# Kernel optimization log

Measured on AMD Instinct MI355X. Metric: run time of the kernel, lower is better.

The kernel has to match this reference:

```python
import jax, jax.numpy as jnp
import numpy as np

N_LEVELS = 16
F_PER_LEVEL = 2
LOG2_T = 19
T = 1 << LOG2_T            # 524288 entries per level
BASE_RES = 16
PER_LEVEL_SCALE = 1.3819
HIDDEN = 64
DIM = 3
PRIMES = (1, 2654435761, 805459861)  # tcnn spatial hash primes

# 8 corner offsets of the unit cube, shape (8, 3)
_CORNERS = np.stack(np.meshgrid(*([np.array([0, 1])] * DIM), indexing='ij'), -1).reshape(-1, DIM)


def hashgrid_encode(x01, table):
    """x01: (N,3) in [0,1]; table: (L, T, F). Returns (N, L*F)."""
    offs = jnp.asarray(_CORNERS, dtype=jnp.int32)          # (8,3)
    offs_u = offs.astype(jnp.uint32)
    feats = []
    for lvl in range(N_LEVELS):
        scale = BASE_RES * (PER_LEVEL_SCALE ** lvl) - 1.0   # grid scale (tcnn convention)
        res = int(np.ceil(scale)) + 1                       # grid resolution for this level
        pos = x01 * jnp.float32(scale) + 0.5
        p0 = jnp.floor(pos)
        w = pos - p0                                        # (N,3) trilinear weights
        p0i = p0.astype(jnp.int32)
        corner = p0i[:, None, :] + offs[None]               # (N,8,3)
        if res ** DIM <= T:
            # dense (coarse) level: linear indexing
            idx = corner[..., 0] + corner[..., 1] * res + corner[..., 2] * (res * res)
        else:
            # fine level: xor spatial hash modulo table size
            c = p0i[:, None, :].astype(jnp.uint32) + offs_u[None]
            h = (c[..., 0] * jnp.uint32(PRIMES[0])) ^ (c[..., 1] * jnp.uint32(PRIMES[1])) ^ (c[..., 2] * jnp.uint32(PRIMES[2]))
            idx = (h & jnp.uint32(T - 1)).astype(jnp.int32)
        cf = table[lvl][idx]                                # (N,8,F) irregular gather
        # trilinear weight per corner: prod over dims of (w if offset==1 else 1-w)
        wmask = jnp.where(offs[None] == 1, w[:, None, :], 1.0 - w[:, None, :])  # (N,8,3)
        wc = jnp.prod(wmask, axis=-1)                       # (N,8)
        feats.append(jnp.sum(cf * wc[..., None], axis=1))   # (N,F)
    return jnp.concatenate(feats, axis=-1)                  # (N, 32)


def _xavier(key, fan_in, fan_out):
    lim = jnp.sqrt(6.0 / (fan_in + fan_out))
    return jax.random.uniform(key, (fan_in, fan_out), jnp.float32, -lim, lim)


def setup_inputs() -> dict:
    key = jax.random.key(0)
    k = jax.random.split(key, 8)
    x = jax.random.uniform(k[0], (1048576, DIM), jnp.float32, -1.0, 1.0)
    # tcnn hashgrid init: uniform(-1e-4, 1e-4)
    table = jax.random.uniform(k[1], (N_LEVELS, T, F_PER_LEVEL), jnp.float32, -1e-4, 1e-4)
    in_dim = N_LEVELS * F_PER_LEVEL
    W1 = _xavier(k[2], in_dim, HIDDEN); b1 = jnp.zeros((HIDDEN,), jnp.float32)
    W2 = _xavier(k[3], HIDDEN, HIDDEN); b2 = jnp.zeros((HIDDEN,), jnp.float32)
    W3 = _xavier(k[4], HIDDEN, 1);      b3 = jnp.zeros((1,), jnp.float32)
    return {"x": x, "table": table, "W1": W1, "b1": b1, "W2": W2, "b2": b2, "W3": W3, "b3": b3}


def reference(x, table, W1, b1, W2, b2, W3, b3):
    x01 = (x + 1.0) * 0.5                       # map [-1,1] -> [0,1]
    enc = hashgrid_encode(x01, table)           # (N, 32)
    h = jax.nn.relu(enc @ W1 + b1)
    h = jax.nn.relu(h @ W2 + b2)
    h = h @ W3 + b3                             # (N, 1), clip_sdf is None
    return h
```

## Files before the change

kernel.cpp:

```cpp
#include <hip/hip_runtime.h>
#include <hip/hip_fp16.h>
#include <cstdint>

#define NTHREADS 256
#define TBL_SIZE (1u << 19)
#define HIDDEN 64
#define NLVL 16
#define PPT 2
#define ENC_SCALE 256.0f
#define ENC_INV (1.0f / 256.0f)

struct Levels { float scale[16]; int res[16]; int dense[16]; };
constexpr Levels make_levels() {
    Levels L{};
    double s = 16.0;
    for (int l = 0; l < 16; ++l) {
        double sc = s - 1.0;
        L.scale[l] = (float)sc;
        int fi = (int)sc;
        int res = fi + (((double)fi < sc) ? 1 : 0) + 1;
        L.res[l] = res;
        L.dense[l] = ((long long)res * res * res <= (long long)TBL_SIZE) ? 1 : 0;
        s *= 1.3819;
    }
    return L;
}
constexpr Levels LV = make_levels();

struct PairOffs { int off[17]; int total; };
constexpr PairOffs make_pairoffs() {
    PairOffs P{}; int o = 0;
    for (int l = 0; l < 16; ++l) {
        P.off[l] = o;
        if (LV.dense[l]) {
            const int r = LV.res[l];
            o += r * (1 + r + r * r) + 2;
        }
    }
    P.off[16] = o; P.total = o;
    return P;
}
constexpr PairOffs PO = make_pairoffs();

#define H16(M) M(0) M(1) M(2) M(3) M(4) M(5) M(6) M(7) \
               M(8) M(9) M(10) M(11) M(12) M(13) M(14) M(15)

typedef _Float16 f16x8 __attribute__((ext_vector_type(8)));
typedef float f32x4 __attribute__((ext_vector_type(4)));

static __device__ __forceinline__ __half2 u32_h2(uint32_t u) {
    union { uint32_t u; __half2 h; } c; c.u = u; return c.h;
}

__global__ __launch_bounds__(256) void cvt_table(const float2* __restrict__ in,
                                                 __half2* __restrict__ out, int n) {
    for (int i = blockIdx.x * 256 + threadIdx.x; i < n; i += gridDim.x * 256) {
        const float2 v = in[i];
        out[i] = __floats2half2_rn(v.x, v.y);
    }
}

__global__ __launch_bounds__(256) void cvt_quads(const __half2* __restrict__ h2,
                                                 uint4* __restrict__ qd) {
    for (int i = blockIdx.x * 256 + threadIdx.x; i < PO.total; i += gridDim.x * 256) {
        int lvl = 0;
        #pragma unroll
        for (int l = 0; l < NLVL; ++l)
            if (LV.dense[l] && i >= PO.off[l] && i < PO.off[l + 1]) lvl = l;
        const int local = i - PO.off[lvl];
        const int res = LV.res[lvl];
        const uint32_t* base = reinterpret_cast<const uint32_t*>(h2 + (size_t)lvl * TBL_SIZE + local);
        uint4 q;
        q.x = base[0];
        q.y = base[1];
        q.z = base[res];
        q.w = base[res + 1];
        qd[i] = q;
    }
}

__global__ __launch_bounds__(256) void cvt_wfrags(const float* __restrict__ W1,
                                                  const float* __restrict__ W2,
                                                  __half* __restrict__ w1f,
                                                  __half* __restrict__ w2f) {
    const int t = blockIdx.x * 256 + threadIdx.x;
    for (int i = t; i < 4 * 64 * 8; i += gridDim.x * 256) {
        const int j = i & 7, lane = (i >> 3) & 63, nt = i >> 9;
        const int k = (lane >> 4) * 8 + j;
        const int o = (lane & 15) + 16 * nt;
        w1f[i] = __float2half(W1[k * HIDDEN + o]);
    }
    for (int i = t; i < 4 * 2 * 64 * 8; i += gridDim.x * 256) {
        const int j = i & 7, lane = (i >> 3) & 63, kb = (i >> 9) & 1, nt = i >> 10;
        const int k = 32 * kb + (lane >> 4) * 8 + j;
        const int o = (lane & 15) + 16 * nt;
        w2f[i] = __float2half(W2[k * HIDDEN + o]);
    }
}

static __device__ __forceinline__ float2 gather_level(
    const __half2* __restrict__ tl, const uint4* __restrict__ qd,
    int dense, int res, int doff,
    int iu, int iv, int iw, float wu, float wv, float ww)
{
    float f0 = 0.0f, f1 = 0.0f;
    const float lx = 1.0f - wu;
    if (dense) {
        const int base = iu + iv * res + iw * res * res;
        #pragma unroll
        for (int o2 = 0; o2 < 2; ++o2) {
            const int idx = base + (o2 ? res * res : 0);
            const uint4 q = qd[doff + idx];
            const float2 a = __half22float2(u32_h2(q.x));
            const float2 b = __half22float2(u32_h2(q.y));
            const float2 c = __half22float2(u32_h2(q.z));
            const float2 d = __half22float2(u32_h2(q.w));
            const float x0l = fmaf(lx, a.x, wu * b.x);
            const float x1l = fmaf(lx, c.x, wu * d.x);
            const float y0l = fmaf(lx, a.y, wu * b.y);
            const float y1l = fmaf(lx, c.y, wu * d.y);
            const float bil0 = fmaf(1.0f - wv, x0l, wv * x1l);
            const float bil1 = fmaf(1.0f - wv, y0l, wv * y1l);
            const float wz = o2 ? ww : 1.0f - ww;
            f0 = fmaf(bil0, wz, f0);
            f1 = fmaf(bil1, wz, f1);
        }
    } else {
        const uint32_t r1a = (uint32_t)iv * 2654435761u;
        const uint32_t r1b = r1a + 2654435761u;
        const uint32_t r2a = (uint32_t)iw * 805459861u;
        const uint32_t r2b = r2a + 805459861u;
        if ((iu & 1) == 0) {
            #pragma unroll
            for (int b4 = 0; b4 < 4; ++b4) {
                const int o1 = (b4 >> 1) & 1, o2 = b4 & 1;
                const uint32_t rest = (o1 ? r1b : r1a) ^ (o2 ? r2b : r2a);
                const uint32_t h0 = ((uint32_t)iu ^ rest) & (TBL_SIZE - 1u);
                const unsigned long long pr =
                    *reinterpret_cast<const unsigned long long*>(tl + (h0 & ~1u));
                const uint32_t lo = (uint32_t)pr, hi = (uint32_t)(pr >> 32);
                const uint32_t sel = h0 & 1u;
                const float2 a = __half22float2(u32_h2(sel ? hi : lo));
                const float2 b = __half22float2(u32_h2(sel ? lo : hi));
                const float wyz = (o1 ? wv : 1.0f - wv) * (o2 ? ww : 1.0f - ww);
                f0 = fmaf(fmaf(lx, a.x, wu * b.x), wyz, f0);
                f1 = fmaf(fmaf(lx, a.y, wu * b.y), wyz, f1);
            }
        } else {
            #pragma unroll
            for (int b4 = 0; b4 < 4; ++b4) {
                const int o1 = (b4 >> 1) & 1, o2 = b4 & 1;
                const uint32_t rest = (o1 ? r1b : r1a) ^ (o2 ? r2b : r2a);
                const uint32_t h0 = ((uint32_t)iu ^ rest) & (TBL_SIZE - 1u);
                const uint32_t h1 = ((uint32_t)(iu + 1) ^ rest) & (TBL_SIZE - 1u);
                const float2 a = __half22float2(tl[h0]);
                const float2 b = __half22float2(tl[h1]);
                const float wyz = (o1 ? wv : 1.0f - wv) * (o2 ? ww : 1.0f - ww);
                f0 = fmaf(fmaf(lx, a.x, wu * b.x), wyz, f0);
                f1 = fmaf(fmaf(lx, a.y, wu * b.y), wyz, f1);
            }
        }
    }
    return make_float2(f0, f1);
}

__global__ __launch_bounds__(NTHREADS, 8) void encode_phased(
    const float* __restrict__ x,
    const __half2* __restrict__ tbl,
    const uint4* __restrict__ qd,
    __half2* __restrict__ enc, int n, int nb)
{
    const int bid = blockIdx.x;
    const int lvl = bid / nb;
    const int pb  = bid - lvl * nb;
    const int i0 = pb * (NTHREADS * PPT) + threadIdx.x;
    const int i1 = i0 + NTHREADS;
    if (i0 >= n) return;

    const float sc = LV.scale[lvl];
    const int res = LV.res[lvl];
    const int dense = LV.dense[lvl];
    const int doff = PO.off[lvl];
    const __half2* tl = tbl + (size_t)lvl * TBL_SIZE;

    const float u0 = (x[3 * i0 + 0] + 1.0f) * 0.5f;
    const float v0 = (x[3 * i0 + 1] + 1.0f) * 0.5f;
    const float w0 = (x[3 * i0 + 2] + 1.0f) * 0.5f;
    const float pu0 = u0 * sc + 0.5f, pv0 = v0 * sc + 0.5f, pw0 = w0 * sc + 0.5f;
    const float fu0 = floorf(pu0), fv0 = floorf(pv0), fw0 = floorf(pw0);

    const bool has1 = (i1 < n);
    const int j1 = has1 ? i1 : i0;
    const float u1 = (x[3 * j1 + 0] + 1.0f) * 0.5f;
    const float v1 = (x[3 * j1 + 1] + 1.0f) * 0.5f;
    const float w1 = (x[3 * j1 + 2] + 1.0f) * 0.5f;
    const float pu1 = u1 * sc + 0.5f, pv1 = v1 * sc + 0.5f, pw1 = w1 * sc + 0.5f;
    const float fu1 = floorf(pu1), fv1 = floorf(pv1), fw1 = floorf(pw1);

    const float2 fA = gather_level(tl, qd, dense, res, doff,
                                   (int)fu0, (int)fv0, (int)fw0,
                                   pu0 - fu0, pv0 - fv0, pw0 - fw0);
    const float2 fB = gather_level(tl, qd, dense, res, doff,
                                   (int)fu1, (int)fv1, (int)fw1,
                                   pu1 - fu1, pv1 - fv1, pw1 - fw1);

    enc[(size_t)lvl * n + i0] = __floats2half2_rn(fA.x * ENC_SCALE, fA.y * ENC_SCALE);
    if (has1) enc[(size_t)lvl * n + i1] = __floats2half2_rn(fB.x * ENC_SCALE, fB.y * ENC_SCALE);
}

__global__ __launch_bounds__(256) void mlp_mfma(
    const __half2* __restrict__ enc,
    const __half* __restrict__ w1f, const __half* __restrict__ w2f,
    const float* __restrict__ b1, const float* __restrict__ b2,
    const float* __restrict__ W3, const float* __restrict__ b3,
    float* __restrict__ out, int n)
{
    __shared__ __half lds_h1[4][64][18];
    const int wid  = threadIdx.x >> 6;
    const int lane = threadIdx.x & 63;
    const int tile = blockIdx.x * 4 + wid;
    const int pt = lane & 15;
    const int qw = lane >> 4;
    const int i = tile * 16 + pt;

    union { uint32_t u[4]; f16x8 v; } bf;
    #pragma unroll
    for (int jj = 0; jj < 4; ++jj)
        bf.u[jj] = *reinterpret_cast<const uint32_t*>(&enc[(size_t)(qw * 4 + jj) * n + i]);

    f32x4 c1[4];
    #pragma unroll
    for (int nt = 0; nt < 4; ++nt) {
        const float4 bb = *(const float4*)&b1[16 * nt + qw * 4];
        c1[nt][0] = bb.x * ENC_SCALE; c1[nt][1] = bb.y * ENC_SCALE;
        c1[nt][2] = bb.z * ENC_SCALE; c1[nt][3] = bb.w * ENC_SCALE;
        const f16x8 a = *reinterpret_cast<const f16x8*>(&w1f[(nt * 64 + lane) * 8]);
        c1[nt] = __builtin_amdgcn_mfma_f32_16x16x32_f16(a, bf.v, c1[nt], 0, 0, 0);
    }

    #pragma unroll
    for (int nt = 0; nt < 4; ++nt) {
        #pragma unroll
        for (int r = 0; r < 4; ++r) {
            const int o = 16 * nt + qw * 4 + r;
            lds_h1[wid][o][pt] = __float2half(fmaxf(c1[nt][r], 0.0f));
        }
    }

    f32x4 c2[4];
    #pragma unroll
    for (int nt = 0; nt < 4; ++nt) {
        const float4 bb = *(const float4*)&b2[16 * nt + qw * 4];
        c2[nt][0] = bb.x * ENC_SCALE; c2[nt][1] = bb.y * ENC_SCALE;
        c2[nt][2] = bb.z * ENC_SCALE; c2[nt][3] = bb.w * ENC_SCALE;
    }
    #pragma unroll
    for (int kb = 0; kb < 2; ++kb) {
        union { uint32_t u[4]; f16x8 v; } hb;
        #pragma unroll
        for (int j2 = 0; j2 < 4; ++j2) {
            const int k0 = kb * 32 + qw * 8 + 2 * j2;
            const uint32_t lo = __half_as_ushort(lds_h1[wid][k0][pt]);
            const uint32_t hi = __half_as_ushort(lds_h1[wid][k0 + 1][pt]);
            hb.u[j2] = lo | (hi << 16);
        }
        #pragma unroll
        for (int nt = 0; nt < 4; ++nt) {
            const f16x8 a = *reinterpret_cast<const f16x8*>(&w2f[((nt * 2 + kb) * 64 + lane) * 8]);
            c2[nt] = __builtin_amdgcn_mfma_f32_16x16x32_f16(a, hb.v, c2[nt], 0, 0, 0);
        }
    }

    float part = 0.0f;
    #pragma unroll
    for (int nt = 0; nt < 4; ++nt) {
        const float4 w3v = *(const float4*)&W3[16 * nt + qw * 4];
        part = fmaf(fmaxf(c2[nt][0], 0.0f), w3v.x, part);
        part = fmaf(fmaxf(c2[nt][1], 0.0f), w3v.y, part);
        part = fmaf(fmaxf(c2[nt][2], 0.0f), w3v.z, part);
        part = fmaf(fmaxf(c2[nt][3], 0.0f), w3v.w, part);
    }
    part += __shfl_xor(part, 16, 64);
    part += __shfl_xor(part, 32, 64);
    if (lane < 16) out[i] = part * ENC_INV + b3[0];
}

__global__ __launch_bounds__(NTHREADS, 4) void mlp_kernel(
    const __half2* __restrict__ enc,
    const float* __restrict__ W1, const float* __restrict__ b1,
    const float* __restrict__ W2, const float* __restrict__ b2,
    const float* __restrict__ W3, const float* __restrict__ b3,
    float* __restrict__ out, int n)
{
    const int i = blockIdx.x * NTHREADS + threadIdx.x;
    if (i >= n) return;

#define DECLH(m) float4 h##m = *(const float4*)&b1[4 * (m)];
    H16(DECLH)
#undef DECLH

    #pragma unroll
    for (int l = 0; l < NLVL; ++l) {
        const float2 f = __half22float2(enc[(size_t)l * n + i]);
        const float f0 = f.x * ENC_INV, f1 = f.y * ENC_INV;
        const float* wra = &W1[(2 * l) * HIDDEN];
        const float* wrb = &W1[(2 * l + 1) * HIDDEN];
#define UPDH(m) { \
        const float4 wa = *(const float4*)&wra[4 * (m)]; \
        const float4 wb = *(const float4*)&wrb[4 * (m)]; \
        h##m.x = fmaf(f0, wa.x, fmaf(f1, wb.x, h##m.x)); \
        h##m.y = fmaf(f0, wa.y, fmaf(f1, wb.y, h##m.y)); \
        h##m.z = fmaf(f0, wa.z, fmaf(f1, wb.z, h##m.z)); \
        h##m.w = fmaf(f0, wa.w, fmaf(f1, wb.w, h##m.w)); }
        H16(UPDH)
#undef UPDH
    }

#define RELUH(m) { h##m.x = fmaxf(h##m.x, 0.0f); h##m.y = fmaxf(h##m.y, 0.0f); \
                   h##m.z = fmaxf(h##m.z, 0.0f); h##m.w = fmaxf(h##m.w, 0.0f); }
    H16(RELUH)
#undef RELUH

    float acc = b3[0];
    #pragma unroll 2
    for (int jb = 0; jb < HIDDEN; jb += 4) {
        float4 t = *(const float4*)&b2[jb];
#define L2K(m) { \
        const float4 r0 = *(const float4*)&W2[(4 * (m) + 0) * HIDDEN + jb]; \
        const float4 r1 = *(const float4*)&W2[(4 * (m) + 1) * HIDDEN + jb]; \
        const float4 r2 = *(const float4*)&W2[(4 * (m) + 2) * HIDDEN + jb]; \
        const float4 r3 = *(const float4*)&W2[(4 * (m) + 3) * HIDDEN + jb]; \
        t.x = fmaf(h##m.x, r0.x, t.x); t.y = fmaf(h##m.x, r0.y, t.y); \
        t.z = fmaf(h##m.x, r0.z, t.z); t.w = fmaf(h##m.x, r0.w, t.w); \
        t.x = fmaf(h##m.y, r1.x, t.x); t.y = fmaf(h##m.y, r1.y, t.y); \
        t.z = fmaf(h##m.y, r1.z, t.z); t.w = fmaf(h##m.y, r1.w, t.w); \
        t.x = fmaf(h##m.z, r2.x, t.x); t.y = fmaf(h##m.z, r2.y, t.y); \
        t.z = fmaf(h##m.z, r2.z, t.z); t.w = fmaf(h##m.z, r2.w, t.w); \
        t.x = fmaf(h##m.w, r3.x, t.x); t.y = fmaf(h##m.w, r3.y, t.y); \
        t.z = fmaf(h##m.w, r3.z, t.z); t.w = fmaf(h##m.w, r3.w, t.w); }
        H16(L2K)
#undef L2K
        const float4 w3v = *(const float4*)&W3[jb];
        acc = fmaf(fmaxf(t.x, 0.0f), w3v.x, acc);
        acc = fmaf(fmaxf(t.y, 0.0f), w3v.y, acc);
        acc = fmaf(fmaxf(t.z, 0.0f), w3v.z, acc);
        acc = fmaf(fmaxf(t.w, 0.0f), w3v.w, acc);
    }

    out[i] = acc;
}

template <bool USE_H2>
__global__ __launch_bounds__(NTHREADS, 4) void sdf_tcnn_fused(
    const float* __restrict__ x,
    const void* __restrict__ tbl,
    const float* __restrict__ W1, const float* __restrict__ b1,
    const float* __restrict__ W2, const float* __restrict__ b2,
    const float* __restrict__ W3, const float* __restrict__ b3,
    float* __restrict__ out, int n)
{
    const int i = blockIdx.x * NTHREADS + threadIdx.x;
    if (i >= n) return;

    const float u = (x[3 * i + 0] + 1.0f) * 0.5f;
    const float v = (x[3 * i + 1] + 1.0f) * 0.5f;
    const float w = (x[3 * i + 2] + 1.0f) * 0.5f;

#define DECLH(m) float4 h##m = *(const float4*)&b1[4 * (m)];
    H16(DECLH)
#undef DECLH

    #pragma unroll
    for (int l = 0; l < NLVL; ++l) {
        const float sc = LV.scale[l];
        const int res = LV.res[l];
        const float pu = u * sc + 0.5f;
        const float pv = v * sc + 0.5f;
        const float pw = w * sc + 0.5f;
        const float fu = floorf(pu), fv = floorf(pv), fw = floorf(pw);
        const float wu = pu - fu, wv = pv - fv, ww = pw - fw;
        const int iu = (int)fu, iv = (int)fv, iw = (int)fw;

        int idx[8];
        #pragma unroll
        for (int b = 0; b < 8; ++b) {
            const int o0 = (b >> 2) & 1, o1 = (b >> 1) & 1, o2 = b & 1;
            if (LV.dense[l]) {
                idx[b] = (iu + o0) + (iv + o1) * res + (iw + o2) * (res * res);
            } else {
                const uint32_t c0 = (uint32_t)(iu + o0);
                const uint32_t c1 = (uint32_t)(iv + o1);
                const uint32_t c2 = (uint32_t)(iw + o2);
                const uint32_t h = c0 ^ (c1 * 2654435761u) ^ (c2 * 805459861u);
                idx[b] = (int)(h & (TBL_SIZE - 1u));
            }
        }

        float f0 = 0.0f, f1 = 0.0f;
        if constexpr (USE_H2) {
            const __half2* tl = (const __half2*)tbl + (size_t)l * TBL_SIZE;
            __half2 cfh[8];
            #pragma unroll
            for (int b = 0; b < 8; ++b) cfh[b] = tl[idx[b]];
            #pragma unroll
            for (int b = 0; b < 8; ++b) {
                const int o0 = (b >> 2) & 1, o1 = (b >> 1) & 1, o2 = b & 1;
                const float wt = (o0 ? wu : 1.0f - wu) *
                                 (o1 ? wv : 1.0f - wv) *
                                 (o2 ? ww : 1.0f - ww);
                const float2 cf = __half22float2(cfh[b]);
                f0 = fmaf(cf.x, wt, f0);
                f1 = fmaf(cf.y, wt, f1);
            }
        } else {
            const float2* tl = (const float2*)tbl + (size_t)l * TBL_SIZE;
            float2 cf[8];
            #pragma unroll
            for (int b = 0; b < 8; ++b) cf[b] = tl[idx[b]];
            #pragma unroll
            for (int b = 0; b < 8; ++b) {
                const int o0 = (b >> 2) & 1, o1 = (b >> 1) & 1, o2 = b & 1;
                const float wt = (o0 ? wu : 1.0f - wu) *
                                 (o1 ? wv : 1.0f - wv) *
                                 (o2 ? ww : 1.0f - ww);
                f0 = fmaf(cf[b].x, wt, f0);
                f1 = fmaf(cf[b].y, wt, f1);
            }
        }

        const float* wra = &W1[(2 * l) * HIDDEN];
        const float* wrb = &W1[(2 * l + 1) * HIDDEN];
#define UPDH(m) { \
        const float4 wa = *(const float4*)&wra[4 * (m)]; \
        const float4 wb = *(const float4*)&wrb[4 * (m)]; \
        h##m.x = fmaf(f0, wa.x, fmaf(f1, wb.x, h##m.x)); \
        h##m.y = fmaf(f0, wa.y, fmaf(f1, wb.y, h##m.y)); \
        h##m.z = fmaf(f0, wa.z, fmaf(f1, wb.z, h##m.z)); \
        h##m.w = fmaf(f0, wa.w, fmaf(f1, wb.w, h##m.w)); }
        H16(UPDH)
#undef UPDH
    }

#define RELUH(m) { h##m.x = fmaxf(h##m.x, 0.0f); h##m.y = fmaxf(h##m.y, 0.0f); \
                   h##m.z = fmaxf(h##m.z, 0.0f); h##m.w = fmaxf(h##m.w, 0.0f); }
    H16(RELUH)
#undef RELUH

    float acc = b3[0];
    #pragma unroll 2
    for (int jb = 0; jb < HIDDEN; jb += 4) {
        float4 t = *(const float4*)&b2[jb];
#define L2K(m) { \
        const float4 r0 = *(const float4*)&W2[(4 * (m) + 0) * HIDDEN + jb]; \
        const float4 r1 = *(const float4*)&W2[(4 * (m) + 1) * HIDDEN + jb]; \
        const float4 r2 = *(const float4*)&W2[(4 * (m) + 2) * HIDDEN + jb]; \
        const float4 r3 = *(const float4*)&W2[(4 * (m) + 3) * HIDDEN + jb]; \
        t.x = fmaf(h##m.x, r0.x, t.x); t.y = fmaf(h##m.x, r0.y, t.y); \
        t.z = fmaf(h##m.x, r0.z, t.z); t.w = fmaf(h##m.x, r0.w, t.w); \
        t.x = fmaf(h##m.y, r1.x, t.x); t.y = fmaf(h##m.y, r1.y, t.y); \
        t.z = fmaf(h##m.y, r1.z, t.z); t.w = fmaf(h##m.y, r1.w, t.w); \
        t.x = fmaf(h##m.z, r2.x, t.x); t.y = fmaf(h##m.z, r2.y, t.y); \
        t.z = fmaf(h##m.z, r2.z, t.z); t.w = fmaf(h##m.z, r2.w, t.w); \
        t.x = fmaf(h##m.w, r3.x, t.x); t.y = fmaf(h##m.w, r3.y, t.y); \
        t.z = fmaf(h##m.w, r3.z, t.z); t.w = fmaf(h##m.w, r3.w, t.w); }
        H16(L2K)
#undef L2K
        const float4 w3v = *(const float4*)&W3[jb];
        acc = fmaf(fmaxf(t.x, 0.0f), w3v.x, acc);
        acc = fmaf(fmaxf(t.y, 0.0f), w3v.y, acc);
        acc = fmaf(fmaxf(t.z, 0.0f), w3v.z, acc);
        acc = fmaf(fmaxf(t.w, 0.0f), w3v.w, acc);
    }

    out[i] = acc;
}

extern "C" void kernel_launch(void* const* d_in, const int* in_sizes, int n_in,
                              void* d_out, int out_size, void* d_ws, size_t ws_size,
                              hipStream_t stream) {
    const float* x     = (const float*)d_in[0];
    const float* table = (const float*)d_in[1];
    const float* W1    = (const float*)d_in[2];
    const float* b1    = (const float*)d_in[3];
    const float* W2    = (const float*)d_in[4];
    const float* b2    = (const float*)d_in[5];
    const float* W3    = (const float*)d_in[6];
    const float* b3    = (const float*)d_in[7];
    float* out = (float*)d_out;

    const int n = in_sizes[0] / 3;
    const int n_entries = NLVL * (int)TBL_SIZE;
    const size_t tbl_bytes   = (size_t)n_entries * sizeof(__half2);
    const size_t quad_bytes  = (size_t)PO.total * 16;
    const size_t wfrag_bytes = 16384;
    const size_t enc_bytes   = (size_t)NLVL * (size_t)n * sizeof(__half2);
    const int nb_mlp = (n + NTHREADS - 1) / NTHREADS;
    const int nb_enc = (n + NTHREADS * PPT - 1) / (NTHREADS * PPT);

    if (ws_size >= tbl_bytes + quad_bytes + wfrag_bytes + enc_bytes) {
        __half2* tbl_h2 = (__half2*)d_ws;
        uint4* qd = (uint4*)((char*)d_ws + tbl_bytes);
        __half* w1f = (__half*)((char*)d_ws + tbl_bytes + quad_bytes);
        __half* w2f = w1f + 4 * 64 * 8;
        __half2* enc = (__half2*)((char*)d_ws + tbl_bytes + quad_bytes + wfrag_bytes);

        hipLaunchKernelGGL(cvt_table, dim3(2048), dim3(256), 0, stream,
                           (const float2*)table, tbl_h2, n_entries);
        hipLaunchKernelGGL(cvt_quads, dim3((PO.total + 255) / 256), dim3(256), 0, stream,
                           tbl_h2, qd);
        hipLaunchKernelGGL(cvt_wfrags, dim3(16), dim3(256), 0, stream,
                           W1, W2, w1f, w2f);
        hipLaunchKernelGGL(encode_phased, dim3(nb_enc * NLVL), dim3(NTHREADS), 0, stream,
                           x, tbl_h2, qd, enc, n, nb_enc);
        if ((n & 63) == 0) {
            hipLaunchKernelGGL(mlp_mfma, dim3(n / 64), dim3(256), 0, stream,
                               enc, w1f, w2f, b1, b2, W3, b3, out, n);
        } else {
            hipLaunchKernelGGL(mlp_kernel, dim3(nb_mlp), dim3(NTHREADS), 0, stream,
                               enc, W1, b1, W2, b2, W3, b3, out, n);
        }
    } else if (ws_size >= tbl_bytes) {
        __half2* tbl_h2 = (__half2*)d_ws;
        hipLaunchKernelGGL(cvt_table, dim3(2048), dim3(256), 0, stream,
                           (const float2*)table, tbl_h2, n_entries);
        hipLaunchKernelGGL((sdf_tcnn_fused<true>), dim3(nb_mlp), dim3(NTHREADS), 0, stream,
                           x, (const void*)tbl_h2, W1, b1, W2, b2, W3, b3, out, n);
    } else {
        hipLaunchKernelGGL((sdf_tcnn_fused<false>), dim3(nb_mlp), dim3(NTHREADS), 0, stream,
                           x, (const void*)table, W1, b1, W2, b2, W3, b3, out, n);
    }
}
```

Before: 334.3 us.

## Split dense and hash level encoding, skip fp16 conversion of dense table levels

Dense levels now get their fp16 corner quads straight from the fp32 table, so the full-table fp16 conversion only covers the hashed levels. The five dense levels are encoded in one kernel that reads each point's coordinates once and loops over levels, while hashed levels keep the per-level phased kernel. The scalar MLP fallback and the intermediate fp16-only fused path are removed, and mlp_mfma is launched with a rounded-up grid even when n is not a multiple of 64. The aim is to cut conversion traffic and launch and x-read overhead, at the cost of an extra launch and fewer blocks for the dense kernel.

```diff
diff --git a/kernel.cpp b/kernel.cpp
--- a/kernel.cpp
+++ b/kernel.cpp
@@ -6,6 +6,8 @@
 #define TBL_SIZE (1u << 19)
 #define HIDDEN 64
 #define NLVL 16
+#define NDENSE 5
+#define NHASH (NLVL - NDENSE)
 #define PPT 2
 #define ENC_SCALE 256.0f
 #define ENC_INV (1.0f / 256.0f)
@@ -26,6 +28,7 @@
     return L;
 }
 constexpr Levels LV = make_levels();
+static_assert(LV.dense[NDENSE - 1] == 1 && LV.dense[NDENSE] == 0, "dense split");
 
 struct PairOffs { int off[17]; int total; };
 constexpr PairOffs make_pairoffs() {
@@ -51,6 +54,9 @@
 static __device__ __forceinline__ __half2 u32_h2(uint32_t u) {
     union { uint32_t u; __half2 h; } c; c.u = u; return c.h;
 }
+static __device__ __forceinline__ uint32_t h2_u32(__half2 h) {
+    union { __half2 h; uint32_t u; } c; c.h = h; return c.u;
+}
 
 __global__ __launch_bounds__(256) void cvt_table(const float2* __restrict__ in,
                                                  __half2* __restrict__ out, int n) {
@@ -60,7 +66,7 @@
     }
 }
 
-__global__ __launch_bounds__(256) void cvt_quads(const __half2* __restrict__ h2,
+__global__ __launch_bounds__(256) void cvt_quads(const float2* __restrict__ tf,
                                                  uint4* __restrict__ qd) {
     for (int i = blockIdx.x * 256 + threadIdx.x; i < PO.total; i += gridDim.x * 256) {
         int lvl = 0;
@@ -69,12 +75,12 @@
             if (LV.dense[l] && i >= PO.off[l] && i < PO.off[l + 1]) lvl = l;
         const int local = i - PO.off[lvl];
         const int res = LV.res[lvl];
-        const uint32_t* base = reinterpret_cast<const uint32_t*>(h2 + (size_t)lvl * TBL_SIZE + local);
+        const float2* base = tf + (size_t)lvl * TBL_SIZE + local;
         uint4 q;
-        q.x = base[0];
-        q.y = base[1];
-        q.z = base[res];
-        q.w = base[res + 1];
+        q.x = h2_u32(__floats2half2_rn(base[0].x, base[0].y));
+        q.y = h2_u32(__floats2half2_rn(base[1].x, base[1].y));
+        q.z = h2_u32(__floats2half2_rn(base[res].x, base[res].y));
+        q.w = h2_u32(__floats2half2_rn(base[res + 1].x, base[res + 1].y));
         qd[i] = q;
     }
 }
@@ -98,89 +104,128 @@
     }
 }
 
-static __device__ __forceinline__ float2 gather_level(
-    const __half2* __restrict__ tl, const uint4* __restrict__ qd,
-    int dense, int res, int doff,
+static __device__ __forceinline__ float2 gather_dense(
+    const uint4* __restrict__ qd, int res, int doff,
     int iu, int iv, int iw, float wu, float wv, float ww)
 {
     float f0 = 0.0f, f1 = 0.0f;
     const float lx = 1.0f - wu;
-    if (dense) {
-        const int base = iu + iv * res + iw * res * res;
-        #pragma unroll
-        for (int o2 = 0; o2 < 2; ++o2) {
-            const int idx = base + (o2 ? res * res : 0);
-            const uint4 q = qd[doff + idx];
-            const float2 a = __half22float2(u32_h2(q.x));
-            const float2 b = __half22float2(u32_h2(q.y));
-            const float2 c = __half22float2(u32_h2(q.z));
-            const float2 d = __half22float2(u32_h2(q.w));
-            const float x0l = fmaf(lx, a.x, wu * b.x);
-            const float x1l = fmaf(lx, c.x, wu * d.x);
-            const float y0l = fmaf(lx, a.y, wu * b.y);
-            const float y1l = fmaf(lx, c.y, wu * d.y);
-            const float bil0 = fmaf(1.0f - wv, x0l, wv * x1l);
-            const float bil1 = fmaf(1.0f - wv, y0l, wv * y1l);
-            const float wz = o2 ? ww : 1.0f - ww;
-            f0 = fmaf(bil0, wz, f0);
-            f1 = fmaf(bil1, wz, f1);
+    const int base = iu + iv * res + iw * res * res;
+    #pragma unroll
+    for (int o2 = 0; o2 < 2; ++o2) {
+        const int idx = base + (o2 ? res * res : 0);
+        const uint4 q = qd[doff + idx];
+        const float2 a = __half22float2(u32_h2(q.x));
+        const float2 b = __half22float2(u32_h2(q.y));
+        const float2 c = __half22float2(u32_h2(q.z));
+        const float2 d = __half22float2(u32_h2(q.w));
+        const float x0l = fmaf(lx, a.x, wu * b.x);
+        const float x1l = fmaf(lx, c.x, wu * d.x);
+        const float y0l = fmaf(lx, a.y, wu * b.y);
+        const float y1l = fmaf(lx, c.y, wu * d.y);
+        const float bil0 = fmaf(1.0f - wv, x0l, wv * x1l);
+        const float bil1 = fmaf(1.0f - wv, y0l, wv * y1l);
+        const float wz = o2 ? ww : 1.0f - ww;
+        f0 = fmaf(bil0, wz, f0);
+        f1 = fmaf(bil1, wz, f1);
+    }
+    return make_float2(f0, f1);
+}
+
+static __device__ __forceinline__ float2 gather_hash(
+    const __half2* __restrict__ tl,
+    int iu, int iv, int iw, float wu, float wv, float ww)
+{
+    float f0 = 0.0f, f1 = 0.0f;
+    const float lx = 1.0f - wu;
+    const uint32_t r1a = (uint32_t)iv * 2654435761u;
+    const uint32_t r1b = r1a + 2654435761u;
+    const uint32_t r2a = (uint32_t)iw * 805459861u;
+    const uint32_t r2b = r2a + 805459861u;
+    if ((iu & 1) == 0) {
+        #pragma unroll
+        for (int b4 = 0; b4 < 4; ++b4) {
+            const int o1 = (b4 >> 1) & 1, o2 = b4 & 1;
+            const uint32_t rest = (o1 ? r1b : r1a) ^ (o2 ? r2b : r2a);
+            const uint32_t h0 = ((uint32_t)iu ^ rest) & (TBL_SIZE - 1u);
+            const unsigned long long pr =
+                *reinterpret_cast<const unsigned long long*>(tl + (h0 & ~1u));
+            const uint32_t lo = (uint32_t)pr, hi = (uint32_t)(pr >> 32);
+            const uint32_t sel = h0 & 1u;
+            const float2 a = __half22float2(u32_h2(sel ? hi : lo));
+            const float2 b = __half22float2(u32_h2(sel ? lo : hi));
+            const float wyz = (o1 ? wv : 1.0f - wv) * (o2 ? ww : 1.0f - ww);
+            f0 = fmaf(fmaf(lx, a.x, wu * b.x), wyz, f0);
+            f1 = fmaf(fmaf(lx, a.y, wu * b.y), wyz, f1);
         }
     } else {
-        const uint32_t r1a = (uint32_t)iv * 2654435761u;
-        const uint32_t r1b = r1a + 2654435761u;
-        const uint32_t r2a = (uint32_t)iw * 805459861u;
-        const uint32_t r2b = r2a + 805459861u;
-        if ((iu & 1) == 0) {
-            #pragma unroll
-            for (int b4 = 0; b4 < 4; ++b4) {
-                const int o1 = (b4 >> 1) & 1, o2 = b4 & 1;
-                const uint32_t rest = (o1 ? r1b : r1a) ^ (o2 ? r2b : r2a);
-                const uint32_t h0 = ((uint32_t)iu ^ rest) & (TBL_SIZE - 1u);
-                const unsigned long long pr =
-                    *reinterpret_cast<const unsigned long long*>(tl + (h0 & ~1u));
-                const uint32_t lo = (uint32_t)pr, hi = (uint32_t)(pr >> 32);
-                const uint32_t sel = h0 & 1u;
-                const float2 a = __half22float2(u32_h2(sel ? hi : lo));
-                const float2 b = __half22float2(u32_h2(sel ? lo : hi));
-                const float wyz = (o1 ? wv : 1.0f - wv) * (o2 ? ww : 1.0f - ww);
-                f0 = fmaf(fmaf(lx, a.x, wu * b.x), wyz, f0);
-                f1 = fmaf(fmaf(lx, a.y, wu * b.y), wyz, f1);
-            }
-        } else {
-            #pragma unroll
-            for (int b4 = 0; b4 < 4; ++b4) {
-                const int o1 = (b4 >> 1) & 1, o2 = b4 & 1;
-                const uint32_t rest = (o1 ? r1b : r1a) ^ (o2 ? r2b : r2a);
-                const uint32_t h0 = ((uint32_t)iu ^ rest) & (TBL_SIZE - 1u);
-                const uint32_t h1 = ((uint32_t)(iu + 1) ^ rest) & (TBL_SIZE - 1u);
-                const float2 a = __half22float2(tl[h0]);
-                const float2 b = __half22float2(tl[h1]);
-                const float wyz = (o1 ? wv : 1.0f - wv) * (o2 ? ww : 1.0f - ww);
-                f0 = fmaf(fmaf(lx, a.x, wu * b.x), wyz, f0);
-                f1 = fmaf(fmaf(lx, a.y, wu * b.y), wyz, f1);
-            }
+        #pragma unroll
+        for (int b4 = 0; b4 < 4; ++b4) {
+            const int o1 = (b4 >> 1) & 1, o2 = b4 & 1;
+            const uint32_t rest = (o1 ? r1b : r1a) ^ (o2 ? r2b : r2a);
+            const uint32_t h0 = ((uint32_t)iu ^ rest) & (TBL_SIZE - 1u);
+            const uint32_t h1 = ((uint32_t)(iu + 1) ^ rest) & (TBL_SIZE - 1u);
+            const float2 a = __half22float2(tl[h0]);
+            const float2 b = __half22float2(tl[h1]);
+            const float wyz = (o1 ? wv : 1.0f - wv) * (o2 ? ww : 1.0f - ww);
+            f0 = fmaf(fmaf(lx, a.x, wu * b.x), wyz, f0);
+            f1 = fmaf(fmaf(lx, a.y, wu * b.y), wyz, f1);
         }
     }
     return make_float2(f0, f1);
 }
 
-__global__ __launch_bounds__(NTHREADS, 8) void encode_phased(
+__global__ __launch_bounds__(NTHREADS, 8) void encode_dense(
+    const float* __restrict__ x,
+    const uint4* __restrict__ qd,
+    __half2* __restrict__ enc, int n)
+{
+    const int i0 = blockIdx.x * (NTHREADS * PPT) + threadIdx.x;
+    const int i1 = i0 + NTHREADS;
+    if (i0 >= n) return;
+
+    const float u0 = (x[3 * i0 + 0] + 1.0f) * 0.5f;
+    const float v0 = (x[3 * i0 + 1] + 1.0f) * 0.5f;
+    const float w0 = (x[3 * i0 + 2] + 1.0f) * 0.5f;
+    const bool has1 = (i1 < n);
+    const int j1 = has1 ? i1 : i0;
+    const float u1 = (x[3 * j1 + 0] + 1.0f) * 0.5f;
+    const float v1 = (x[3 * j1 + 1] + 1.0f) * 0.5f;
+    const float w1 = (x[3 * j1 + 2] + 1.0f) * 0.5f;
+
+    #pragma unroll
+    for (int l = 0; l < NDENSE; ++l) {
+        const float sc = LV.scale[l];
+        const int res = LV.res[l];
+        const int doff = PO.off[l];
+
+        const float pu0 = u0 * sc + 0.5f, pv0 = v0 * sc + 0.5f, pw0 = w0 * sc + 0.5f;
+        const float fu0 = floorf(pu0), fv0 = floorf(pv0), fw0 = floorf(pw0);
+        const float2 fA = gather_dense(qd, res, doff, (int)fu0, (int)fv0, (int)fw0,
+                                       pu0 - fu0, pv0 - fv0, pw0 - fw0);
+        const float pu1 = u1 * sc + 0.5f, pv1 = v1 * sc + 0.5f, pw1 = w1 * sc + 0.5f;
+        const float fu1 = floorf(pu1), fv1 = floorf(pv1), fw1 = floorf(pw1);
+        const float2 fB = gather_dense(qd, res, doff, (int)fu1, (int)fv1, (int)fw1,
+                                       pu1 - fu1, pv1 - fv1, pw1 - fw1);
+
+        enc[(size_t)l * n + i0] = __floats2half2_rn(fA.x * ENC_SCALE, fA.y * ENC_SCALE);
+        if (has1) enc[(size_t)l * n + i1] = __floats2half2_rn(fB.x * ENC_SCALE, fB.y * ENC_SCALE);
+    }
+}
+
+__global__ __launch_bounds__(NTHREADS, 8) void encode_hash(
     const float* __restrict__ x,
     const __half2* __restrict__ tbl,
-    const uint4* __restrict__ qd,
     __half2* __restrict__ enc, int n, int nb)
 {
     const int bid = blockIdx.x;
-    const int lvl = bid / nb;
-    const int pb  = bid - lvl * nb;
+    const int lvl = NDENSE + bid / nb;
+    const int pb  = bid - (lvl - NDENSE) * nb;
     const int i0 = pb * (NTHREADS * PPT) + threadIdx.x;
     const int i1 = i0 + NTHREADS;
     if (i0 >= n) return;
 
     const float sc = LV.scale[lvl];
-    const int res = LV.res[lvl];
-    const int dense = LV.dense[lvl];
-    const int doff = PO.off[lvl];
     const __half2* tl = tbl + (size_t)lvl * TBL_SIZE;
 
     const float u0 = (x[3 * i0 + 0] + 1.0f) * 0.5f;
@@ -197,12 +242,10 @@
     const float pu1 = u1 * sc + 0.5f, pv1 = v1 * sc + 0.5f, pw1 = w1 * sc + 0.5f;
     const float fu1 = floorf(pu1), fv1 = floorf(pv1), fw1 = floorf(pw1);
 
-    const float2 fA = gather_level(tl, qd, dense, res, doff,
-                                   (int)fu0, (int)fv0, (int)fw0,
-                                   pu0 - fu0, pv0 - fv0, pw0 - fw0);
-    const float2 fB = gather_level(tl, qd, dense, res, doff,
-                                   (int)fu1, (int)fv1, (int)fw1,
-                                   pu1 - fu1, pv1 - fv1, pw1 - fw1);
+    const float2 fA = gather_hash(tl, (int)fu0, (int)fv0, (int)fw0,
+                                  pu0 - fu0, pv0 - fv0, pw0 - fw0);
+    const float2 fB = gather_hash(tl, (int)fu1, (int)fv1, (int)fw1,
+                                  pu1 - fu1, pv1 - fv1, pw1 - fw1);
 
     enc[(size_t)lvl * n + i0] = __floats2half2_rn(fA.x * ENC_SCALE, fA.y * ENC_SCALE);
     if (has1) enc[(size_t)lvl * n + i1] = __floats2half2_rn(fB.x * ENC_SCALE, fB.y * ENC_SCALE);
@@ -283,71 +326,6 @@
     part += __shfl_xor(part, 16, 64);
     part += __shfl_xor(part, 32, 64);
     if (lane < 16) out[i] = part * ENC_INV + b3[0];
-}
-
-__global__ __launch_bounds__(NTHREADS, 4) void mlp_kernel(
-    const __half2* __restrict__ enc,
-    const float* __restrict__ W1, const float* __restrict__ b1,
-    const float* __restrict__ W2, const float* __restrict__ b2,
-    const float* __restrict__ W3, const float* __restrict__ b3,
-    float* __restrict__ out, int n)
-{
-    const int i = blockIdx.x * NTHREADS + threadIdx.x;
-    if (i >= n) return;
-
-#define DECLH(m) float4 h##m = *(const float4*)&b1[4 * (m)];
-    H16(DECLH)
-#undef DECLH
-
-    #pragma unroll
-    for (int l = 0; l < NLVL; ++l) {
-        const float2 f = __half22float2(enc[(size_t)l * n + i]);
-        const float f0 = f.x * ENC_INV, f1 = f.y * ENC_INV;
-        const float* wra = &W1[(2 * l) * HIDDEN];
-        const float* wrb = &W1[(2 * l + 1) * HIDDEN];
-#define UPDH(m) { \
-        const float4 wa = *(const float4*)&wra[4 * (m)]; \
-        const float4 wb = *(const float4*)&wrb[4 * (m)]; \
-        h##m.x = fmaf(f0, wa.x, fmaf(f1, wb.x, h##m.x)); \
-        h##m.y = fmaf(f0, wa.y, fmaf(f1, wb.y, h##m.y)); \
-        h##m.z = fmaf(f0, wa.z, fmaf(f1, wb.z, h##m.z)); \
-        h##m.w = fmaf(f0, wa.w, fmaf(f1, wb.w, h##m.w)); }
-        H16(UPDH)
-#undef UPDH
-    }
-
-#define RELUH(m) { h##m.x = fmaxf(h##m.x, 0.0f); h##m.y = fmaxf(h##m.y, 0.0f); \
-                   h##m.z = fmaxf(h##m.z, 0.0f); h##m.w = fmaxf(h##m.w, 0.0f); }
-    H16(RELUH)
-#undef RELUH
-
-    float acc = b3[0];
-    #pragma unroll 2
-    for (int jb = 0; jb < HIDDEN; jb += 4) {
-        float4 t = *(const float4*)&b2[jb];
-#define L2K(m) { \
-        const float4 r0 = *(const float4*)&W2[(4 * (m) + 0) * HIDDEN + jb]; \
-        const float4 r1 = *(const float4*)&W2[(4 * (m) + 1) * HIDDEN + jb]; \
-        const float4 r2 = *(const float4*)&W2[(4 * (m) + 2) * HIDDEN + jb]; \
-        const float4 r3 = *(const float4*)&W2[(4 * (m) + 3) * HIDDEN + jb]; \
-        t.x = fmaf(h##m.x, r0.x, t.x); t.y = fmaf(h##m.x, r0.y, t.y); \
-        t.z = fmaf(h##m.x, r0.z, t.z); t.w = fmaf(h##m.x, r0.w, t.w); \
-        t.x = fmaf(h##m.y, r1.x, t.x); t.y = fmaf(h##m.y, r1.y, t.y); \
-        t.z = fmaf(h##m.y, r1.z, t.z); t.w = fmaf(h##m.y, r1.w, t.w); \
-        t.x = fmaf(h##m.z, r2.x, t.x); t.y = fmaf(h##m.z, r2.y, t.y); \
-        t.z = fmaf(h##m.z, r2.z, t.z); t.w = fmaf(h##m.z, r2.w, t.w); \
-        t.x = fmaf(h##m.w, r3.x, t.x); t.y = fmaf(h##m.w, r3.y, t.y); \
-        t.z = fmaf(h##m.w, r3.z, t.z); t.w = fmaf(h##m.w, r3.w, t.w); }
-        H16(L2K)
-#undef L2K
-        const float4 w3v = *(const float4*)&W3[jb];
-        acc = fmaf(fmaxf(t.x, 0.0f), w3v.x, acc);
-        acc = fmaf(fmaxf(t.y, 0.0f), w3v.y, acc);
-        acc = fmaf(fmaxf(t.z, 0.0f), w3v.z, acc);
-        acc = fmaf(fmaxf(t.w, 0.0f), w3v.w, acc);
-    }
-
-    out[i] = acc;
 }
 
 template <bool USE_H2>
@@ -505,26 +483,19 @@
         __half2* enc = (__half2*)((char*)d_ws + tbl_bytes + quad_bytes + wfrag_bytes);
 
         hipLaunchKernelGGL(cvt_table, dim3(2048), dim3(256), 0, stream,
-                           (const float2*)table, tbl_h2, n_entries);
+                           (const float2*)table + (size_t)NDENSE * TBL_SIZE,
+                           tbl_h2 + (size_t)NDENSE * TBL_SIZE,
+                           NHASH * (int)TBL_SIZE);
         hipLaunchKernelGGL(cvt_quads, dim3((PO.total + 255) / 256), dim3(256), 0, stream,
-                           tbl_h2, qd);
+                           (const float2*)table, qd);
         hipLaunchKernelGGL(cvt_wfrags, dim3(16), dim3(256), 0, stream,
                            W1, W2, w1f, w2f);
-        hipLaunchKernelGGL(encode_phased, dim3(nb_enc * NLVL), dim3(NTHREADS), 0, stream,
-                           x, tbl_h2, qd, enc, n, nb_enc);
-        if ((n & 63) == 0) {
-            hipLaunchKernelGGL(mlp_mfma, dim3(n / 64), dim3(256), 0, stream,
-                               enc, w1f, w2f, b1, b2, W3, b3, out, n);
-        } else {
-            hipLaunchKernelGGL(mlp_kernel, dim3(nb_mlp), dim3(NTHREADS), 0, stream,
-                               enc, W1, b1, W2, b2, W3, b3, out, n);
-        }
-    } else if (ws_size >= tbl_bytes) {
-        __half2* tbl_h2 = (__half2*)d_ws;
-        hipLaunchKernelGGL(cvt_table, dim3(2048), dim3(256), 0, stream,
-                           (const float2*)table, tbl_h2, n_entries);
-        hipLaunchKernelGGL((sdf_tcnn_fused<true>), dim3(nb_mlp), dim3(NTHREADS), 0, stream,
-                           x, (const void*)tbl_h2, W1, b1, W2, b2, W3, b3, out, n);
+        hipLaunchKernelGGL(encode_dense, dim3(nb_enc), dim3(NTHREADS), 0, stream,
+                           x, qd, enc, n);
+        hipLaunchKernelGGL(encode_hash, dim3(nb_enc * NHASH), dim3(NTHREADS), 0, stream,
+                           x, tbl_h2, enc, n, nb_enc);
+        hipLaunchKernelGGL(mlp_mfma, dim3((n + 63) / 64), dim3(256), 0, stream,
+                           enc, w1f, w2f, b1, b2, W3, b3, out, n);
     } else {
         hipLaunchKernelGGL((sdf_tcnn_fused<false>), dim3(nb_mlp), dim3(NTHREADS), 0, stream,
                            x, (const void*)table, W1, b1, W2, b2, W3, b3, out, n);
```

New measurement: 321.1 us. 4.0% less time.
